# Performance work log

Measured on AMD Instinct MI355X. Metric: run time of the kernel, lower is better.

Reference implementation:

```python
import jax, jax.numpy as jnp
import numpy as np

B, S, D, H = 4, 2048, 1024, 16
HD = D // H


def setup_inputs() -> dict:
    key = jax.random.key(0)
    ks = jax.random.split(key, 12)
    sc = 0.02
    inp = {
        "q": jax.random.normal(ks[0], (B, S, D), jnp.float32),
        "k": jax.random.normal(ks[1], (B, S, D), jnp.float32),
        "v": jax.random.normal(ks[2], (B, S, D), jnp.float32),
        "mask": jnp.tril(jnp.ones((S, S), jnp.int32))[None, None],  # causal [1,1,S,S]
        "Wq": jax.random.normal(ks[3], (D, D), jnp.float32) * sc,
        "bq": jnp.zeros((D,), jnp.float32),
        "Wk": jax.random.normal(ks[4], (D, D), jnp.float32) * sc,
        "bk": jnp.zeros((D,), jnp.float32),
        "Wv": jax.random.normal(ks[5], (D, D), jnp.float32) * sc,
        "bv": jnp.zeros((D,), jnp.float32),
        "Wo": jax.random.normal(ks[6], (D, D), jnp.float32) * sc,
        "bo": jnp.zeros((D,), jnp.float32),
    }
    return inp


def reference(q, k, v, mask, Wq, bq, Wk, bk, Wv, bv, Wo, bo):
    # Linear projections (torch Linear: x @ W.T + b)
    qh = (q @ Wq.T + bq).reshape(B, S, H, HD).transpose(0, 2, 1, 3)  # [B,H,S,hd]
    kh = (k @ Wk.T + bk).reshape(B, S, H, HD).transpose(0, 2, 1, 3)
    vh = (v @ Wv.T + bv).reshape(B, S, H, HD).transpose(0, 2, 1, 3)
    score = jnp.einsum("bhqd,bhkd->bhqk", qh, kh) / jnp.sqrt(jnp.float32(HD))
    score = jnp.where(mask == 0, jnp.float32(-10000.0), score)
    attn = jax.nn.softmax(score, axis=-1)
    out = jnp.einsum("bhqk,bhkd->bhqd", attn, vh)  # [B,H,S,hd]
    out = out.transpose(0, 2, 1, 3).reshape(B, S, D)
    return out @ Wo.T + bo
```

## Files before the change

kernel.cpp:

```cpp
#include <hip/hip_runtime.h>

#define S_LEN 2048
#define D_DIM 1024
#define NB    4
#define NH    16
#define HDIM  64
#define QSCL  0.18033688011112042f

typedef float  f32x4  __attribute__((ext_vector_type(4)));
typedef __bf16 bf16x4 __attribute__((ext_vector_type(4)));
typedef __bf16 bf16x8 __attribute__((ext_vector_type(8)));

static __device__ __forceinline__ f32x4 mfma16(bf16x8 a, bf16x8 b, f32x4 c) {
  return __builtin_amdgcn_mfma_f32_16x16x32_bf16(a, b, c, 0, 0, 0);
}
static __device__ __forceinline__ bf16x4 cvt4(f32x4 v) {
  return __builtin_convertvector(v, bf16x4);
}
static __device__ __forceinline__ void cp16(const void* g, void* l) {
  __builtin_amdgcn_global_load_lds(
      (const __attribute__((address_space(1))) unsigned int*)g,
      (__attribute__((address_space(3))) unsigned int*)l, 16, 0, 0);
}

__global__ __launch_bounds__(256) void conv_all(
    const float* __restrict__ q, const float* __restrict__ k,
    const float* __restrict__ v,
    const float* __restrict__ Wq, const float* __restrict__ Wk,
    const float* __restrict__ Wv, const float* __restrict__ Wo,
    __bf16* __restrict__ abf, __bf16* __restrict__ wbf)
{
  const int y = blockIdx.y;
  if (y < 3) {
    const float* src = (y == 0) ? q : (y == 1) ? k : v;
    size_t i = ((size_t)blockIdx.x * 256 + threadIdx.x) * 4;
    f32x4 x = *(const f32x4*)(src + i);
    *(bf16x4*)(abf + (size_t)y * ((size_t)NB * S_LEN * D_DIM) + i) = cvt4(x);
  } else {
    if (blockIdx.x >= 4096) return;
    const int w = blockIdx.x >> 10;
    const float* src = (w == 0) ? Wq : (w == 1) ? Wk : (w == 2) ? Wv : Wo;
    size_t i = ((size_t)(blockIdx.x & 1023) * 256 + threadIdx.x) * 4;
    f32x4 x = *(const f32x4*)(src + i);
    *(bf16x4*)(wbf + (size_t)w * (D_DIM * D_DIM) + i) = cvt4(x);
  }
}

static __device__ __forceinline__ void proj_epilogue(
    f32x4 (&acc)[4][4], int z, int mbase, int nbase, int wm, int wn,
    int l15, int quad, const float* bias,
    __bf16* qh, __bf16* kh, __bf16* vt)
{
  const float scl = (z == 0) ? QSCL : 1.0f;
#pragma unroll
  for (int mt = 0; mt < 4; ++mt)
#pragma unroll
    for (int nt = 0; nt < 4; ++nt) {
      int n = nbase + wn + nt * 16 + l15;
      int h = n >> 6, hd = n & 63;
      float bb = bias[n];
      f32x4 vv = acc[mt][nt];
#pragma unroll
      for (int r = 0; r < 4; ++r) vv[r] = (vv[r] + bb) * scl;
      bf16x4 pv = cvt4(vv);
      int m0 = mbase + wm + mt * 16 + quad * 4;
      int b = m0 >> 11, s0 = m0 & 2047;
      if (z == 2) {
        *(bf16x4*)(vt + ((size_t)((b * NH + h) * HDIM + hd)) * S_LEN + s0) = pv;
      } else {
        __bf16* out = (z == 0) ? qh : kh;
#pragma unroll
        for (int r = 0; r < 4; ++r)
          out[((size_t)(b * NH + h) * S_LEN + s0 + r) * HDIM + hd] = pv[r];
      }
    }
}

__global__ __launch_bounds__(256, 4) void proj_bf16(
    const __bf16* __restrict__ abf, const __bf16* __restrict__ Wbf,
    const float* __restrict__ bq, const float* __restrict__ bk, const float* __restrict__ bv,
    __bf16* __restrict__ qh, __bf16* __restrict__ kh, __bf16* __restrict__ vt)
{
  const int lin = blockIdx.x + (blockIdx.y << 6) + (blockIdx.z << 9);
  const int wg  = (lin & 7) * 192 + (lin >> 3);
  const int z   = wg >> 9;
  const int rem = wg & 511;
  const int xg  = rem >> 3;
  const int yg  = rem & 7;

  const __bf16* A = abf + (size_t)z * ((size_t)NB * S_LEN * D_DIM);
  const __bf16* W = Wbf + (size_t)z * (D_DIM * D_DIM);
  const float* bias = (z == 0) ? bq : (z == 1) ? bk : bv;

  __shared__ __bf16 As[128 * 64];
  __shared__ __bf16 Bs[128 * 64];

  const int tid  = threadIdx.x;
  const int wave = tid >> 6;
  const int lane = tid & 63;
  const int l15  = lane & 15;
  const int quad = lane >> 4;
  const int mbase = xg * 128;
  const int nbase = yg * 128;
  const int wm = (wave & 1) * 64;
  const int wn = (wave >> 1) * 64;
  const int brow = lane >> 3;
  const int scol = ((lane & 7) ^ (brow & 7)) * 8;
  const int swz  = l15 & 7;

  f32x4 acc[4][4] = {};

  for (int kt = 0; kt < D_DIM; kt += 64) {
#pragma unroll
    for (int c = 0; c < 4; ++c) {
      int r = wave * 32 + c * 8 + brow;
      cp16(A + (size_t)(mbase + r) * D_DIM + kt + scol, As + r * 64);
      cp16(W + (size_t)(nbase + r) * D_DIM + kt + scol, Bs + r * 64);
    }
    __syncthreads();

#pragma unroll
    for (int k0 = 0; k0 < 2; ++k0) {
      bf16x8 af[4], bfr[4];
#pragma unroll
      for (int i = 0; i < 4; ++i) {
        int off = ((k0 * 4 + quad) ^ swz) * 8;
        af[i]  = *(const bf16x8*)(As + (wm + i * 16 + l15) * 64 + off);
        bfr[i] = *(const bf16x8*)(Bs + (wn + i * 16 + l15) * 64 + off);
      }
#pragma unroll
      for (int mt = 0; mt < 4; ++mt)
#pragma unroll
        for (int nt = 0; nt < 4; ++nt)
          acc[mt][nt] = mfma16(af[mt], bfr[nt], acc[mt][nt]);
    }
    __syncthreads();
  }

  proj_epilogue(acc, z, mbase, nbase, wm, wn, l15, quad, bias, qh, kh, vt);
}

__global__ __launch_bounds__(256, 4) void attn_kernel(
    const __bf16* __restrict__ qh, const __bf16* __restrict__ kh,
    const __bf16* __restrict__ vt, __bf16* __restrict__ ao)
{
  __shared__ __bf16 Kb[2][64 * 64];
  __shared__ __bf16 Vb[2][64 * 64];

  const int lin = blockIdx.x + (blockIdx.y << 4);
  const int xcd = lin & 7;
  const int idx = lin >> 3;
  const int u   = idx & 15;
  const int x   = (u & 1) ? (15 - (u >> 1)) : (u >> 1);
  const int bh  = xcd * 8 + (idx >> 4);

  const int qc0 = x, qc1 = 31 - x;
  const int last = qc1;

  const __bf16* qp = qh + (size_t)bh * S_LEN * HDIM;
  const __bf16* kp = kh + (size_t)bh * S_LEN * HDIM;
  const __bf16* vp = vt + (size_t)bh * HDIM * S_LEN;

  const int tid  = threadIdx.x;
  const int wave = tid >> 6;
  const int lane = tid & 63;
  const int l15  = lane & 15;
  const int quad = lane >> 4;
  const int w16  = wave * 16;
  const int srow = lane >> 3;
  const int swz  = l15 & 7;
  const int vswz = ((l15 >> 3) << 2) | (l15 & 3);
  const int kr0  = ((l15 >> 2) << 3) | (l15 & 3);
  const int b = bh >> 4, h = bh & 15;

  bf16x8 fq[2][2];
#pragma unroll
  for (int j = 0; j < 2; ++j) {
    const int qb = (j ? qc1 : qc0) * 64;
    const __bf16* qrow = qp + (size_t)(qb + w16 + l15) * HDIM;
    fq[j][0] = *(const bf16x8*)(qrow + quad * 8);
    fq[j][1] = *(const bf16x8*)(qrow + 32 + quad * 8);
  }

  f32x4 accO[2][4] = {};
  float lp[2] = {0.f, 0.f};

#pragma unroll
  for (int c = 0; c < 2; ++c) {
    int rb = w16 + c * 8;
    int sc2 = (((lane & 7) ^ (((c & 1) << 2) | (srow & 3)))) * 8;
    cp16(kp + (size_t)(rb + srow) * HDIM + sc2, &Kb[0][rb * 64]);
    cp16(vp + (size_t)(rb + srow) * S_LEN + sc2, &Vb[0][rb * 64]);
  }

  int cur = 0;
  for (int kt = 0; kt <= last; ++kt) {
    __syncthreads();

    if (kt < last) {
#pragma unroll
      for (int c = 0; c < 2; ++c) {
        int rb = w16 + c * 8;
        int sc2 = (((lane & 7) ^ (((c & 1) << 2) | (srow & 3)))) * 8;
        cp16(kp + (size_t)((kt + 1) * 64 + rb + srow) * HDIM + sc2,
             &Kb[cur ^ 1][rb * 64]);
        cp16(vp + (size_t)(rb + srow) * S_LEN + (kt + 1) * 64 + sc2,
             &Vb[cur ^ 1][rb * 64]);
      }
    }

    const __bf16* Kc = &Kb[cur][0];
    const __bf16* Vc = &Vb[cur][0];
    const bool act0 = (kt <= qc0);

    f32x4 sc[2][4] = {};
    __builtin_amdgcn_s_setprio(1);
#pragma unroll
    for (int k0 = 0; k0 < 2; ++k0)
#pragma unroll
      for (int nt = 0; nt < 4; ++nt) {
        const int krow = kr0 + ((nt & 1) << 2) + ((nt >> 1) << 5);
        bf16x8 bk = *(const bf16x8*)(Kc + krow * 64 +
                                     (((k0 * 4 + quad) ^ swz) * 8));
        if (act0) sc[0][nt] = mfma16(bk, fq[0][k0], sc[0][nt]);
        sc[1][nt] = mfma16(bk, fq[1][k0], sc[1][nt]);
      }
    __builtin_amdgcn_s_setprio(0);

    bf16x8 pa[2][2];
#pragma unroll
    for (int j = 0; j < 2; ++j) {
      if (j == 0 && !act0) continue;
      const int qcj = j ? qc1 : qc0;
      f32x4 pf[4];
#pragma unroll
      for (int nt = 0; nt < 4; ++nt) {
#pragma unroll
        for (int r = 0; r < 4; ++r) pf[nt][r] = __builtin_amdgcn_exp2f(sc[j][nt][r]);
        if (kt == qcj) {
#pragma unroll
          for (int r = 0; r < 4; ++r) {
            int key = ((nt >> 1) << 5) + (quad << 3) + ((nt & 1) << 2) + r;
            if (key > w16 + l15) pf[nt][r] = 0.f;
          }
        }
      }
      f32x4 lv = (pf[0] + pf[1]) + (pf[2] + pf[3]);
      lp[j] += (lv[0] + lv[1]) + (lv[2] + lv[3]);
      bf16x4 c0 = cvt4(pf[0]), c1 = cvt4(pf[1]), c2 = cvt4(pf[2]), c3 = cvt4(pf[3]);
      bf16x8 p0, p1;
      p0[0]=c0[0]; p0[1]=c0[1]; p0[2]=c0[2]; p0[3]=c0[3];
      p0[4]=c1[0]; p0[5]=c1[1]; p0[6]=c1[2]; p0[7]=c1[3];
      p1[0]=c2[0]; p1[1]=c2[1]; p1[2]=c2[2]; p1[3]=c2[3];
      p1[4]=c3[0]; p1[5]=c3[1]; p1[6]=c3[2]; p1[7]=c3[3];
      pa[j][0] = p0;
      pa[j][1] = p1;
    }

    __builtin_amdgcn_s_setprio(1);
#pragma unroll
    for (int k0 = 0; k0 < 2; ++k0)
#pragma unroll
      for (int nt = 0; nt < 4; ++nt) {
        bf16x8 bv = *(const bf16x8*)(Vc + (nt * 16 + l15) * 64 +
                                     (((k0 * 4 + quad) ^ vswz) * 8));
        if (act0) accO[0][nt] = mfma16(pa[0][k0], bv, accO[0][nt]);
        accO[1][nt] = mfma16(pa[1][k0], bv, accO[1][nt]);
      }
    __builtin_amdgcn_s_setprio(0);

    cur ^= 1;
  }

#pragma unroll
  for (int j = 0; j < 2; ++j) {
    float lf = lp[j];
    lf += __shfl_xor(lf, 16);
    lf += __shfl_xor(lf, 32);
    const int qb = (j ? qc1 : qc0) * 64;
#pragma unroll
    for (int r = 0; r < 4; ++r) {
      float inv = 1.0f / __shfl(lf, quad * 4 + r);
#pragma unroll
      for (int nt = 0; nt < 4; ++nt) accO[j][nt][r] *= inv;
    }
#pragma unroll
    for (int nt = 0; nt < 4; ++nt) {
      bf16x4 ob = cvt4(accO[j][nt]);
#pragma unroll
      for (int r = 0; r < 4; ++r) {
        int sr = qb + w16 + quad * 4 + r;
        ao[((size_t)b * S_LEN + sr) * D_DIM + h * HDIM + nt * 16 + l15] = ob[r];
      }
    }
  }
}

__global__ __launch_bounds__(256, 4) void out_gemm(
    const __bf16* __restrict__ Ain, const __bf16* __restrict__ Wbf,
    const float* __restrict__ bo, float* __restrict__ Cout)
{
  const int lin = blockIdx.x + (blockIdx.y << 6);
  const int wg  = (lin & 7) * 64 + (lin >> 3);
  const int xg  = wg >> 3;
  const int yg  = wg & 7;

  __shared__ __bf16 As[128 * 64];
  __shared__ __bf16 Bs[128 * 64];

  const int tid  = threadIdx.x;
  const int wave = tid >> 6;
  const int lane = tid & 63;
  const int l15  = lane & 15;
  const int quad = lane >> 4;
  const int mbase = xg * 128;
  const int nbase = yg * 128;
  const int wm = (wave & 1) * 64;
  const int wn = (wave >> 1) * 64;
  const int brow = lane >> 3;
  const int scol = ((lane & 7) ^ (brow & 7)) * 8;
  const int swz  = l15 & 7;

  f32x4 acc[4][4] = {};

  for (int kt = 0; kt < D_DIM; kt += 64) {
#pragma unroll
    for (int c = 0; c < 4; ++c) {
      int r = wave * 32 + c * 8 + brow;
      cp16(Ain + (size_t)(mbase + r) * D_DIM + kt + scol, As + r * 64);
      cp16(Wbf + (size_t)(nbase + r) * D_DIM + kt + scol, Bs + r * 64);
    }
    __syncthreads();

#pragma unroll
    for (int k0 = 0; k0 < 2; ++k0) {
      bf16x8 af[4], bfr[4];
#pragma unroll
      for (int i = 0; i < 4; ++i) {
        int off = ((k0 * 4 + quad) ^ swz) * 8;
        af[i]  = *(const bf16x8*)(As + (wm + i * 16 + l15) * 64 + off);
        bfr[i] = *(const bf16x8*)(Bs + (wn + i * 16 + l15) * 64 + off);
      }
#pragma unroll
      for (int mt = 0; mt < 4; ++mt)
#pragma unroll
        for (int nt = 0; nt < 4; ++nt)
          acc[mt][nt] = mfma16(af[mt], bfr[nt], acc[mt][nt]);
    }
    __syncthreads();
  }

#pragma unroll
  for (int mt = 0; mt < 4; ++mt)
#pragma unroll
    for (int nt = 0; nt < 4; ++nt) {
      int n = nbase + wn + nt * 16 + l15;
      float bb = bo[n];
      int m0 = mbase + wm + mt * 16 + quad * 4;
#pragma unroll
      for (int r = 0; r < 4; ++r)
        Cout[(size_t)(m0 + r) * D_DIM + n] = acc[mt][nt][r] + bb;
    }
}

extern "C" void kernel_launch(void* const* d_in, const int* in_sizes, int n_in,
                              void* d_out, int out_size, void* d_ws, size_t ws_size,
                              hipStream_t stream) {
  const float* q  = (const float*)d_in[0];
  const float* k  = (const float*)d_in[1];
  const float* v  = (const float*)d_in[2];
  const float* Wq = (const float*)d_in[4];
  const float* bq = (const float*)d_in[5];
  const float* Wk = (const float*)d_in[6];
  const float* bk = (const float*)d_in[7];
  const float* Wv = (const float*)d_in[8];
  const float* bv = (const float*)d_in[9];
  const float* Wo = (const float*)d_in[10];
  const float* bo = (const float*)d_in[11];

  __bf16* ws = (__bf16*)d_ws;
  const size_t WSZ = (size_t)D_DIM * D_DIM;
  const size_t NE  = (size_t)NB * S_LEN * D_DIM;
  __bf16* wbf = ws;
  __bf16* qh  = ws + 4 * WSZ;
  __bf16* kh  = qh + NE;
  __bf16* vt  = kh + NE;
  __bf16* ao  = vt + NE;
  __bf16* abf = vt + NE;

  conv_all<<<dim3(8192, 4), 256, 0, stream>>>(q, k, v, Wq, Wk, Wv, Wo, abf, wbf);
  proj_bf16<<<dim3(64, 8, 3), 256, 0, stream>>>(abf, wbf, bq, bk, bv, qh, kh, vt);
  attn_kernel<<<dim3(16, 64), 256, 0, stream>>>(qh, kh, vt, ao);
  out_gemm<<<dim3(64, 8), 256, 0, stream>>>(ao, wbf + 3 * WSZ, bo, (float*)d_out);
}
```

Before: 300.4 us.

## Process four query tiles per attention block to reuse K/V tiles

Each attention workgroup now handles four 64-row query chunks (two balanced causal pairs) instead of two. Every K/V tile loaded into LDS therefore feeds twice as many query tiles, which halves the K/V global loads per head. The grid is halved and launch bounds drop to 2 waves per SIMD to leave room for the doubled accumulator and Q-fragment registers. The cost is lower occupancy and fewer blocks (512), which could leave CUs underused or hurt latency hiding.

```diff
diff --git a/kernel.cpp b/kernel.cpp
--- a/kernel.cpp
+++ b/kernel.cpp
@@ -140,22 +140,21 @@
   proj_epilogue(acc, z, mbase, nbase, wm, wn, l15, quad, bias, qh, kh, vt);
 }
 
-__global__ __launch_bounds__(256, 4) void attn_kernel(
+__global__ __launch_bounds__(256, 2) void attn_kernel(
     const __bf16* __restrict__ qh, const __bf16* __restrict__ kh,
     const __bf16* __restrict__ vt, __bf16* __restrict__ ao)
 {
   __shared__ __bf16 Kb[2][64 * 64];
   __shared__ __bf16 Vb[2][64 * 64];
 
-  const int lin = blockIdx.x + (blockIdx.y << 4);
+  const int lin = blockIdx.x + (blockIdx.y << 3);
   const int xcd = lin & 7;
   const int idx = lin >> 3;
-  const int u   = idx & 15;
-  const int x   = (u & 1) ? (15 - (u >> 1)) : (u >> 1);
-  const int bh  = xcd * 8 + (idx >> 4);
-
-  const int qc0 = x, qc1 = 31 - x;
-  const int last = qc1;
+  const int x   = idx & 7;
+  const int bh  = xcd * 8 + (idx >> 3);
+
+  const int qcs[4] = { x, 31 - x, x + 8, 23 - x };
+  const int last = 31 - x;
 
   const __bf16* qp = qh + (size_t)bh * S_LEN * HDIM;
   const __bf16* kp = kh + (size_t)bh * S_LEN * HDIM;
@@ -173,17 +172,17 @@
   const int kr0  = ((l15 >> 2) << 3) | (l15 & 3);
   const int b = bh >> 4, h = bh & 15;
 
-  bf16x8 fq[2][2];
-#pragma unroll
-  for (int j = 0; j < 2; ++j) {
-    const int qb = (j ? qc1 : qc0) * 64;
+  bf16x8 fq[4][2];
+#pragma unroll
+  for (int j = 0; j < 4; ++j) {
+    const int qb = qcs[j] * 64;
     const __bf16* qrow = qp + (size_t)(qb + w16 + l15) * HDIM;
     fq[j][0] = *(const bf16x8*)(qrow + quad * 8);
     fq[j][1] = *(const bf16x8*)(qrow + 32 + quad * 8);
   }
 
-  f32x4 accO[2][4] = {};
-  float lp[2] = {0.f, 0.f};
+  f32x4 accO[4][4] = {};
+  float lp[4] = {0.f, 0.f, 0.f, 0.f};
 
 #pragma unroll
   for (int c = 0; c < 2; ++c) {
@@ -211,73 +210,81 @@
 
     const __bf16* Kc = &Kb[cur][0];
     const __bf16* Vc = &Vb[cur][0];
-    const bool act0 = (kt <= qc0);
-
-    f32x4 sc[2][4] = {};
-    __builtin_amdgcn_s_setprio(1);
-#pragma unroll
-    for (int k0 = 0; k0 < 2; ++k0)
-#pragma unroll
-      for (int nt = 0; nt < 4; ++nt) {
-        const int krow = kr0 + ((nt & 1) << 2) + ((nt >> 1) << 5);
-        bf16x8 bk = *(const bf16x8*)(Kc + krow * 64 +
-                                     (((k0 * 4 + quad) ^ swz) * 8));
-        if (act0) sc[0][nt] = mfma16(bk, fq[0][k0], sc[0][nt]);
-        sc[1][nt] = mfma16(bk, fq[1][k0], sc[1][nt]);
-      }
-    __builtin_amdgcn_s_setprio(0);
-
-    bf16x8 pa[2][2];
-#pragma unroll
-    for (int j = 0; j < 2; ++j) {
-      if (j == 0 && !act0) continue;
-      const int qcj = j ? qc1 : qc0;
-      f32x4 pf[4];
-#pragma unroll
-      for (int nt = 0; nt < 4; ++nt) {
-#pragma unroll
-        for (int r = 0; r < 4; ++r) pf[nt][r] = __builtin_amdgcn_exp2f(sc[j][nt][r]);
-        if (kt == qcj) {
-#pragma unroll
-          for (int r = 0; r < 4; ++r) {
-            int key = ((nt >> 1) << 5) + (quad << 3) + ((nt & 1) << 2) + r;
-            if (key > w16 + l15) pf[nt][r] = 0.f;
+    const bool skip1 = (kt > 23 - x);
+
+#pragma unroll
+    for (int p = 0; p < 2; ++p) {
+      if (p == 1 && skip1) continue;
+      const int ja = 2 * p, jb = 2 * p + 1;
+      const bool actA = (kt <= qcs[ja]);
+
+      f32x4 sc[2][4] = {};
+      __builtin_amdgcn_s_setprio(1);
+#pragma unroll
+      for (int k0 = 0; k0 < 2; ++k0)
+#pragma unroll
+        for (int nt = 0; nt < 4; ++nt) {
+          const int krow = kr0 + ((nt & 1) << 2) + ((nt >> 1) << 5);
+          bf16x8 bk = *(const bf16x8*)(Kc + krow * 64 +
+                                       (((k0 * 4 + quad) ^ swz) * 8));
+          if (actA) sc[0][nt] = mfma16(bk, fq[ja][k0], sc[0][nt]);
+          sc[1][nt] = mfma16(bk, fq[jb][k0], sc[1][nt]);
+        }
+      __builtin_amdgcn_s_setprio(0);
+
+      bf16x8 pa[2][2];
+#pragma unroll
+      for (int jj = 0; jj < 2; ++jj) {
+        if (jj == 0 && !actA) continue;
+        const int j = 2 * p + jj;
+        const int qcj = qcs[j];
+        f32x4 pf[4];
+#pragma unroll
+        for (int nt = 0; nt < 4; ++nt) {
+#pragma unroll
+          for (int r = 0; r < 4; ++r) pf[nt][r] = __builtin_amdgcn_exp2f(sc[jj][nt][r]);
+          if (kt == qcj) {
+#pragma unroll
+            for (int r = 0; r < 4; ++r) {
+              int key = ((nt >> 1) << 5) + (quad << 3) + ((nt & 1) << 2) + r;
+              if (key > w16 + l15) pf[nt][r] = 0.f;
+            }
           }
         }
-      }
-      f32x4 lv = (pf[0] + pf[1]) + (pf[2] + pf[3]);
-      lp[j] += (lv[0] + lv[1]) + (lv[2] + lv[3]);
-      bf16x4 c0 = cvt4(pf[0]), c1 = cvt4(pf[1]), c2 = cvt4(pf[2]), c3 = cvt4(pf[3]);
-      bf16x8 p0, p1;
-      p0[0]=c0[0]; p0[1]=c0[1]; p0[2]=c0[2]; p0[3]=c0[3];
-      p0[4]=c1[0]; p0[5]=c1[1]; p0[6]=c1[2]; p0[7]=c1[3];
-      p1[0]=c2[0]; p1[1]=c2[1]; p1[2]=c2[2]; p1[3]=c2[3];
-      p1[4]=c3[0]; p1[5]=c3[1]; p1[6]=c3[2]; p1[7]=c3[3];
-      pa[j][0] = p0;
-      pa[j][1] = p1;
-    }
-
-    __builtin_amdgcn_s_setprio(1);
-#pragma unroll
-    for (int k0 = 0; k0 < 2; ++k0)
-#pragma unroll
-      for (int nt = 0; nt < 4; ++nt) {
-        bf16x8 bv = *(const bf16x8*)(Vc + (nt * 16 + l15) * 64 +
-                                     (((k0 * 4 + quad) ^ vswz) * 8));
-        if (act0) accO[0][nt] = mfma16(pa[0][k0], bv, accO[0][nt]);
-        accO[1][nt] = mfma16(pa[1][k0], bv, accO[1][nt]);
-      }
-    __builtin_amdgcn_s_setprio(0);
+        f32x4 lv = (pf[0] + pf[1]) + (pf[2] + pf[3]);
+        lp[j] += (lv[0] + lv[1]) + (lv[2] + lv[3]);
+        bf16x4 c0 = cvt4(pf[0]), c1 = cvt4(pf[1]), c2 = cvt4(pf[2]), c3 = cvt4(pf[3]);
+        bf16x8 p0, p1;
+        p0[0]=c0[0]; p0[1]=c0[1]; p0[2]=c0[2]; p0[3]=c0[3];
+        p0[4]=c1[0]; p0[5]=c1[1]; p0[6]=c1[2]; p0[7]=c1[3];
+        p1[0]=c2[0]; p1[1]=c2[1]; p1[2]=c2[2]; p1[3]=c2[3];
+        p1[4]=c3[0]; p1[5]=c3[1]; p1[6]=c3[2]; p1[7]=c3[3];
+        pa[jj][0] = p0;
+        pa[jj][1] = p1;
+      }
+
+      __builtin_amdgcn_s_setprio(1);
+#pragma unroll
+      for (int k0 = 0; k0 < 2; ++k0)
+#pragma unroll
+        for (int nt = 0; nt < 4; ++nt) {
+          bf16x8 bv = *(const bf16x8*)(Vc + (nt * 16 + l15) * 64 +
+                                       (((k0 * 4 + quad) ^ vswz) * 8));
+          if (actA) accO[ja][nt] = mfma16(pa[0][k0], bv, accO[ja][nt]);
+          accO[jb][nt] = mfma16(pa[1][k0], bv, accO[jb][nt]);
+        }
+      __builtin_amdgcn_s_setprio(0);
+    }
 
     cur ^= 1;
   }
 
 #pragma unroll
-  for (int j = 0; j < 2; ++j) {
+  for (int j = 0; j < 4; ++j) {
     float lf = lp[j];
     lf += __shfl_xor(lf, 16);
     lf += __shfl_xor(lf, 32);
-    const int qb = (j ? qc1 : qc0) * 64;
+    const int qb = qcs[j] * 64;
 #pragma unroll
     for (int r = 0; r < 4; ++r) {
       float inv = 1.0f / __shfl(lf, quad * 4 + r);
@@ -390,6 +397,6 @@
 
   conv_all<<<dim3(8192, 4), 256, 0, stream>>>(q, k, v, Wq, Wk, Wv, Wo, abf, wbf);
   proj_bf16<<<dim3(64, 8, 3), 256, 0, stream>>>(abf, wbf, bq, bk, bv, qh, kh, vt);
-  attn_kernel<<<dim3(16, 64), 256, 0, stream>>>(qh, kh, vt, ao);
+  attn_kernel<<<dim3(8, 64), 256, 0, stream>>>(qh, kh, vt, ao);
   out_gemm<<<dim3(64, 8), 256, 0, stream>>>(ao, wbf + 3 * WSZ, bo, (float*)d_out);
 }
```

Measured after the change: 319.1 us. +6.2%, slower.
